# Performance work log

Hardware: AMD Instinct MI355X
Metric: run time of the kernel (lower is better)

The kernel has to match this reference:

```python
import math
import jax, jax.numpy as jnp
import numpy as np

B, N, D, H = 2, 2048, 1024, 16
HD = D // H  # 64
TWO_PI = 2.0 * math.pi
ROPE_BASE = 10000.0


def setup_inputs() -> dict:
    key = jax.random.key(0)
    ks = jax.random.split(key, 8)
    s = 0.02
    x = jax.random.normal(ks[0], (B, N, D), dtype=jnp.float32)
    Wq = jax.random.normal(ks[1], (D, D), dtype=jnp.float32) * s
    Wk = jax.random.normal(ks[2], (D, D), dtype=jnp.float32) * s
    Wv = jax.random.normal(ks[3], (D, D), dtype=jnp.float32) * s
    Wo = jax.random.normal(ks[4], (D, D), dtype=jnp.float32) * s
    cw = jax.random.normal(ks[5], (D,), dtype=jnp.float32) * s  # complexity_proj weight
    cb = jnp.zeros((), dtype=jnp.float32)                        # complexity_proj bias
    alpha = jnp.asarray(0.1, dtype=jnp.float32)
    T_base = jnp.asarray(10.0, dtype=jnp.float32)
    root_ids = jax.random.randint(ks[6], (B, N), 0, 1000)
    mask = jnp.tril(jnp.ones((N, N), dtype=jnp.int32))  # causal
    return {"x": x, "Wq": Wq, "Wk": Wk, "Wv": Wv, "Wo": Wo,
            "alpha": alpha, "T_base": T_base, "cw": cw, "cb": cb,
            "root_ids": root_ids, "mask": mask, "t_step": 3}


def _rope_cos_sin(seq_len, head_dim, dtype):
    inv_freq = 1.0 / (ROPE_BASE ** (jnp.arange(0, head_dim, 2, dtype=jnp.float32) / head_dim))
    pos = jnp.arange(seq_len, dtype=jnp.float32)
    freqs = pos[:, None] * inv_freq[None, :]          # (N, HD/2)
    emb = jnp.concatenate([freqs, freqs], axis=-1)    # (N, HD)
    return jnp.cos(emb).astype(dtype), jnp.sin(emb).astype(dtype)


def _rotate_half(t):
    half = t.shape[-1] // 2
    return jnp.concatenate([-t[..., half:], t[..., :half]], axis=-1)


def reference(x, Wq, Wk, Wv, Wo, alpha, T_base, cw, cb, root_ids, mask, t_step):
    b, n, d = x.shape
    # QKV projection -> (B, H, N, HD)
    def proj(W):
        return jnp.einsum('bnd,ed->bne', x, W).reshape(b, n, H, HD).transpose(0, 2, 1, 3)
    q, k, v = proj(Wq), proj(Wk), proj(Wv)
    # RoPE
    cos, sin = _rope_cos_sin(n, HD, x.dtype)          # (N, HD)
    q = q * cos + _rotate_half(q) * sin
    k = k * cos + _rotate_half(k) * sin
    # Per-sample temperature via complexity + cardiac oscillation
    complexity = jax.nn.sigmoid(jnp.einsum('bd,d->b', x.mean(axis=1), cw) + cb)  # (B,)
    T_eff = (jnp.abs(T_base) + 1.0) * (0.5 + complexity)                          # (B,)
    psi = 1.0 + alpha * jnp.sin(TWO_PI * t_step / T_eff)                          # (B,)
    scale = (math.sqrt(HD) * psi)[:, None, None, None]                            # (B,1,1,1)
    # Attention with full NxN scores (eager path, as in source)
    scores = jnp.einsum('bhqd,bhkd->bhqk', q, k) / scale
    scores = jnp.where(mask[None, None, :, :] == 0, -jnp.inf, scores)
    attn = jax.nn.softmax(scores, axis=-1)
    out = jnp.einsum('bhqk,bhkd->bhqd', attn, v)       # (B,H,N,HD)
    out = out.transpose(0, 2, 1, 3).reshape(b, n, d)
    return jnp.einsum('bnd,ed->bne', out, Wo)
```

## Files before the change

### kernel.cpp

```cpp
#include <hip/hip_runtime.h>


typedef short short8 __attribute__((ext_vector_type(8)));
typedef float floatx4 __attribute__((ext_vector_type(4)));
typedef float f32x16 __attribute__((ext_vector_type(16)));
typedef unsigned int uint4v __attribute__((ext_vector_type(4)));
typedef unsigned int u32x4v __attribute__((ext_vector_type(4)));
typedef unsigned short us4 __attribute__((ext_vector_type(4)));
typedef unsigned short u16;

#define DEV __device__ __forceinline__

static const int Bb = 2;

static const size_t OFF_XB = 0;
static const size_t OFF_WQ = 8388608;
static const size_t OFF_WK = OFF_WQ + 2097152;
static const size_t OFF_WV = OFF_WK + 2097152;
static const size_t OFF_WO = OFF_WV + 2097152;
static const size_t OFF_Q  = OFF_WO + 2097152;
static const size_t OFF_K  = OFF_Q + 8388608;
static const size_t OFF_V  = OFF_K + 8388608;
static const size_t OFF_AO = OFF_V + 8388608;
static const size_t OFF_SC = OFF_AO + 8388608;

DEV u16 f2bf(float f) {
  unsigned int u = __builtin_bit_cast(unsigned int, f);
  u += 0x7fffu + ((u >> 16) & 1u);
  return (u16)(u >> 16);
}

DEV unsigned pkbf(float lo, float hi) {
  unsigned r;
  asm("v_cvt_pk_bf16_f32 %0, %1, %2" : "=v"(r) : "v"(lo), "v"(hi));
  return r;
}

__global__ __launch_bounds__(256) void cvt_all_kernel(
    const float* __restrict__ x, const float* __restrict__ wq,
    const float* __restrict__ wk, const float* __restrict__ wv,
    const float* __restrict__ wo, const float* __restrict__ cw,
    u16* __restrict__ xb, u16* __restrict__ wqb, u16* __restrict__ wkb,
    u16* __restrict__ wvb, u16* __restrict__ wob, float* __restrict__ part) {
  const int blk = blockIdx.x;
  if (blk < 4096) {
    int i = blk * 256 + threadIdx.x;
    float4 f = ((const float4*)x)[i];
    us4 o;
    o[0] = f2bf(f.x); o[1] = f2bf(f.y); o[2] = f2bf(f.z); o[3] = f2bf(f.w);
    ((us4*)xb)[i] = o;
    float4 c = ((const float4*)cw)[i & 255];
    float acc = f.x * c.x + f.y * c.y + f.z * c.z + f.w * c.w;
    __shared__ float red[256];
    red[threadIdx.x] = acc;
    __syncthreads();
    for (int s = 128; s > 0; s >>= 1) {
      if (threadIdx.x < s) red[threadIdx.x] += red[threadIdx.x + s];
      __syncthreads();
    }
    if (threadIdx.x == 0) part[blk] = red[0];
  } else {
    int r = blk - 4096;
    int wi = r >> 10;
    int i = (r & 1023) * 256 + threadIdx.x;
    const float* src = (wi == 0) ? wq : (wi == 1) ? wk : (wi == 2) ? wv : wo;
    u16* dst = (wi == 0) ? wqb : (wi == 1) ? wkb : (wi == 2) ? wvb : wob;
    float4 f = ((const float4*)src)[i];
    us4 o;
    o[0] = f2bf(f.x); o[1] = f2bf(f.y); o[2] = f2bf(f.z); o[3] = f2bf(f.w);
    ((us4*)dst)[i] = o;
  }
}

__global__ void prep_kernel(const float* __restrict__ part,
                            const float* __restrict__ cb,
                            const float* __restrict__ alpha,
                            const float* __restrict__ tb,
                            const int* __restrict__ tstep,
                            float* __restrict__ out, float2* __restrict__ rt) {
  if (blockIdx.x == 256) {
    const int b = threadIdx.x >> 7, t = threadIdx.x & 127;
    float s = 0.f;
    for (int i = t; i < 2048; i += 128) s += part[b * 2048 + i];
    __shared__ float red[2][128];
    red[b][t] = s;
    __syncthreads();
    for (int st = 64; st > 0; st >>= 1) {
      if (t < st) red[b][t] += red[b][t + st];
      __syncthreads();
    }
    if (t == 0) {
      float sm = red[b][0] * (1.0f / 2048.0f) + cb[0];
      float cx = 1.0f / (1.0f + expf(-sm));
      float Te = (fabsf(tb[0]) + 1.0f) * (0.5f + cx);
      float psi = 1.0f + alpha[0] * sinf(6.283185307179586f * (float)tstep[0] / Te);
      out[b] = 1.0f / (8.0f * psi);
    }
  } else {
    int i = blockIdx.x * 256 + threadIdx.x;
    int pos = i >> 5, hd2 = i & 31;
    float ang = (float)pos * exp2f(-(float)hd2 * 0.41524101186092030f);
    float sv, cv;
    sincosf(ang, &sv, &cv);
    rt[i] = make_float2(cv, sv);
  }
}

__global__ __launch_bounds__(256) void gemm_qkv_kernel(
    const u16* __restrict__ xb, const u16* __restrict__ wq, const u16* __restrict__ wk,
    const u16* __restrict__ wv, const float2* __restrict__ rt,
    u16* __restrict__ q, u16* __restrict__ k, u16* __restrict__ v) {
  const int tm = blockIdx.x, tn = blockIdx.y, which = blockIdx.z;
  const u16* W = (which == 0) ? wq : (which == 1) ? wk : wv;
  u16* dst = (which == 0) ? q : (which == 1) ? k : v;

  __shared__ __align__(16) u16 As[128 * 32];
  __shared__ __align__(16) u16 Bs[128 * 32];

  const int t = threadIdx.x, lane = t & 63, w = t >> 6;
  const int wm = w >> 1, wn = w & 1, lg = lane >> 4, lr = lane & 15;

  floatx4 acc[4][4];
#pragma unroll
  for (int i = 0; i < 4; i++)
#pragma unroll
    for (int j = 0; j < 4; j++) acc[i][j] = (floatx4){0.f, 0.f, 0.f, 0.f};

  const int rowA = tm * 128, rowB = tn * 128;
  for (int kt = 0; kt < 32; ++kt) {
#pragma unroll
    for (int s = 0; s < 2; s++) {
      int c = t + s * 256;
      int r = c >> 2, kc = c & 3;
      *(uint4v*)(As + r * 32 + kc * 8) =
          *(const uint4v*)(xb + (size_t)(rowA + r) * 1024 + kt * 32 + kc * 8);
      *(uint4v*)(Bs + r * 32 + kc * 8) =
          *(const uint4v*)(W + (size_t)(rowB + r) * 1024 + kt * 32 + kc * 8);
    }
    __syncthreads();
    short8 af[4], bw[4];
#pragma unroll
    for (int i = 0; i < 4; i++)
      af[i] = *(const short8*)(As + (wm * 64 + i * 16 + lr) * 32 + lg * 8);
#pragma unroll
    for (int j = 0; j < 4; j++)
      bw[j] = *(const short8*)(Bs + (wn * 64 + j * 16 + lr) * 32 + lg * 8);
#pragma unroll
    for (int i = 0; i < 4; i++)
#pragma unroll
      for (int j = 0; j < 4; j++)
        acc[i][j] = __builtin_amdgcn_mfma_f32_16x16x32_bf16(af[i], bw[j], acc[i][j], 0, 0, 0);
    __syncthreads();
  }

  const int rowbase = tm * 128 + wm * 64, colbase = tn * 128 + wn * 64;
  if (which <= 1) {
#pragma unroll
    for (int i = 0; i < 4; i++)
#pragma unroll
      for (int ii = 0; ii < 4; ii++) {
        int gm = rowbase + i * 16 + lg * 4 + ii;
        int pos = gm & 2047, bb = gm >> 11;
#pragma unroll
        for (int jp = 0; jp < 2; jp++) {
          int hd2 = jp * 16 + lr;
          float2 cs = rt[pos * 32 + hd2];
          float a0 = acc[i][jp][ii], a1 = acc[i][jp + 2][ii];
          int e0 = colbase + jp * 16 + lr;
          int hh = e0 >> 6;
          size_t base = (((size_t)bb * 16 + hh) * 2048 + pos) * 64;
          dst[base + hd2]      = f2bf(a0 * cs.x - a1 * cs.y);
          dst[base + hd2 + 32] = f2bf(a1 * cs.x + a0 * cs.y);
        }
      }
  } else {
#pragma unroll
    for (int i = 0; i < 4; i++)
#pragma unroll
      for (int ii = 0; ii < 4; ii++) {
        int gm = rowbase + i * 16 + lg * 4 + ii;
        int pos = gm & 2047, bb = gm >> 11;
#pragma unroll
        for (int j = 0; j < 4; j++) {
          int ge = colbase + j * 16 + lr;
          int hh = ge >> 6, hd = ge & 63;
          dst[(((size_t)bb * 16 + hh) * 2048 + pos) * 64 + hd] = f2bf(acc[i][j][ii]);
        }
      }
  }
}

__global__ __launch_bounds__(256) void vtrans_kernel(const u16* __restrict__ v,
                                                     u16* __restrict__ vt) {
  const int bh = blockIdx.x, nt = blockIdx.y;
  __shared__ __align__(16) u16 T[64 * 64];
  const int t = threadIdx.x;
  const size_t vi = (size_t)bh * 131072 + (size_t)nt * 4096;
#pragma unroll
  for (int s = 0; s < 2; s++) {
    int g = s * 256 + t, n = g >> 3, dc = g & 7;
    *(uint4v*)(T + n * 64 + ((dc ^ (n & 7)) * 8)) =
        *(const uint4v*)(v + vi + (size_t)n * 64 + dc * 8);
  }
  __syncthreads();
  const size_t vo = (size_t)bh * 131072 + (size_t)nt * 64;
#pragma unroll
  for (int s = 0; s < 2; s++) {
    int g = s * 256 + t, nc = g & 7, d = g >> 3;
    short8 o;
#pragma unroll
    for (int jj = 0; jj < 8; jj++) {
      int n = nc * 8 + jj;
      o[jj] = (short)T[n * 64 + (((d >> 3) ^ (n & 7)) * 8) + (d & 7)];
    }
    *(short8*)(vt + vo + (size_t)d * 2048 + nc * 8) = o;
  }
}

__global__ __launch_bounds__(256) void attn_kernel(
    const u16* __restrict__ q, const u16* __restrict__ k, const u16* __restrict__ vt,
    u16* __restrict__ ao, const float* __restrict__ scale_ws) {
  const int bid = blockIdx.x;
  const int swz = (bid & 7) * 64 + (bid >> 3);
  const int bh = swz >> 4, p = swz & 15;
  const int b = bh >> 4, h = bh & 15;
  const int w = threadIdx.x >> 6, lane = threadIdx.x & 63;
  const int l31 = lane & 31, hi = lane >> 5;
  const int tsel = (w == 0) ? p : (w == 1) ? 31 - p : (w == 2) ? 32 + p : 63 - p;
  const int q0 = tsel * 32;
  const int KT = tsel >> 1;
  const float isc2 = scale_ws[b] * 1.4426950408889634f;
  const size_t koff = (size_t)bh * 131072;
  const float NINF = -__builtin_inff();

  short8 bq[4];
#pragma unroll
  for (int k4 = 0; k4 < 4; k4++)
    bq[k4] = *(const short8*)(q + koff + (size_t)(q0 + l31) * 64 + k4 * 16 + hi * 8);

  f32x16 o0, o1;
#pragma unroll
  for (int r = 0; r < 16; r++) { o0[r] = 0.f; o1[r] = 0.f; }
  float m2 = NINF, ell = 0.f;

  for (int kt = 0; kt <= KT; ++kt) {
    const int cbase = kt << 6;
    const bool haveMt1 = (cbase + 32 <= q0 + 31);

    short8 ka0[4], ka1[4];
#pragma unroll
    for (int k4 = 0; k4 < 4; k4++)
      ka0[k4] = *(const short8*)(k + koff + (size_t)(cbase + l31) * 64 + k4 * 16 + hi * 8);
    if (haveMt1) {
#pragma unroll
      for (int k4 = 0; k4 < 4; k4++)
        ka1[k4] = *(const short8*)(k + koff + (size_t)(cbase + 32 + l31) * 64 + k4 * 16 + hi * 8);
    }
    const int nct = haveMt1 ? 4 : 2;
    short8 va0[4], va1[4];
#pragma unroll
    for (int ct = 0; ct < 4; ct++) {
      if (ct < nct) {
        va0[ct] = *(const short8*)(vt + koff + (size_t)l31 * 2048 + cbase + ct * 16 + hi * 8);
        va1[ct] = *(const short8*)(vt + koff + (size_t)(32 + l31) * 2048 + cbase + ct * 16 + hi * 8);
      }
    }

    f32x16 s0, s1;
#pragma unroll
    for (int r = 0; r < 16; r++) { s0[r] = 0.f; s1[r] = 0.f; }
    __builtin_amdgcn_s_setprio(1);
#pragma unroll
    for (int k4 = 0; k4 < 4; k4++)
      s0 = __builtin_amdgcn_mfma_f32_32x32x16_bf16(ka0[k4], bq[k4], s0, 0, 0, 0);
    if (haveMt1) {
#pragma unroll
      for (int k4 = 0; k4 < 4; k4++)
        s1 = __builtin_amdgcn_mfma_f32_32x32x16_bf16(ka1[k4], bq[k4], s1, 0, 0, 0);
    }
    __builtin_amdgcn_s_setprio(0);

#pragma unroll
    for (int r = 0; r < 16; r++) { s0[r] *= isc2; s1[r] *= isc2; }
    if (kt == KT) {
      const int thr = q0 + l31 - cbase;
#pragma unroll
      for (int r = 0; r < 16; r++) {
        const int crow = (r & 3) + 8 * (r >> 2) + 4 * hi;
        if (crow > thr) s0[r] = NINF;
        if (crow + 32 > thr) s1[r] = NINF;
      }
    }

    float mx = s0[0];
#pragma unroll
    for (int r = 1; r < 16; r++) mx = fmaxf(mx, s0[r]);
#pragma unroll
    for (int r = 0; r < 16; r++) mx = fmaxf(mx, s1[r]);
    mx = fmaxf(mx, __shfl_xor(mx, 32, 64));
    if (!__all(mx <= m2 + 8.0f)) {
      const float mn = fmaxf(m2, mx);
      const float rsc = exp2f(m2 - mn);
      m2 = mn;
      ell *= rsc;
#pragma unroll
      for (int r = 0; r < 16; r++) { o0[r] *= rsc; o1[r] *= rsc; }
    }
    f32x16 p0, p1;
    float ps = 0.f;
#pragma unroll
    for (int r = 0; r < 16; r++) { p0[r] = exp2f(s0[r] - m2); ps += p0[r]; }
#pragma unroll
    for (int r = 0; r < 16; r++) { p1[r] = exp2f(s1[r] - m2); ps += p1[r]; }
    ps += __shfl_xor(ps, 32, 64);
    ell += ps;

    __builtin_amdgcn_s_setprio(1);
#pragma unroll
    for (int ct = 0; ct < 4; ct++) {
      if (ct < nct) {
        const f32x16& pp = (ct < 2) ? p0 : p1;
        const int rA = (ct & 1) * 8;
        unsigned pkA0 = pkbf(pp[rA + 0], pp[rA + 1]);
        unsigned pkA1 = pkbf(pp[rA + 2], pp[rA + 3]);
        unsigned pkB0 = pkbf(pp[rA + 4], pp[rA + 5]);
        unsigned pkB1 = pkbf(pp[rA + 6], pp[rA + 7]);
        unsigned u0 = (unsigned)__shfl_xor((int)(hi ? pkA0 : pkB0), 32, 64);
        unsigned u1 = (unsigned)__shfl_xor((int)(hi ? pkA1 : pkB1), 32, 64);
        u32x4v pu;
        pu[0] = hi ? u0 : pkA0;
        pu[1] = hi ? u1 : pkA1;
        pu[2] = hi ? pkB0 : u0;
        pu[3] = hi ? pkB1 : u1;
        short8 pf = __builtin_bit_cast(short8, pu);
        o0 = __builtin_amdgcn_mfma_f32_32x32x16_bf16(va0[ct], pf, o0, 0, 0, 0);
        o1 = __builtin_amdgcn_mfma_f32_32x32x16_bf16(va1[ct], pf, o1, 0, 0, 0);
      }
    }
    __builtin_amdgcn_s_setprio(0);
  }

  const float invl = 1.0f / ell;
  u16* orow = ao + ((size_t)(b * 2048 + q0 + l31)) * 1024 + h * 64;
#pragma unroll
  for (int qd = 0; qd < 4; qd++) {
    us4 st0, st1;
#pragma unroll
    for (int j = 0; j < 4; j++) {
      st0[j] = f2bf(o0[qd * 4 + j] * invl);
      st1[j] = f2bf(o1[qd * 4 + j] * invl);
    }
    *(us4*)(orow + qd * 8 + hi * 4) = st0;
    *(us4*)(orow + 32 + qd * 8 + hi * 4) = st1;
  }
}

__global__ __launch_bounds__(256) void gemm_out_kernel(const u16* __restrict__ ab,
                                                       const u16* __restrict__ wo,
                                                       float* __restrict__ out) {
  const int tm = blockIdx.x, tn = blockIdx.y;
  __shared__ __align__(16) u16 As[128 * 32];
  __shared__ __align__(16) u16 Bs[128 * 32];

  const int t = threadIdx.x, lane = t & 63, w = t >> 6;
  const int wm = w >> 1, wn = w & 1, lg = lane >> 4, lr = lane & 15;

  floatx4 acc[4][4];
#pragma unroll
  for (int i = 0; i < 4; i++)
#pragma unroll
    for (int j = 0; j < 4; j++) acc[i][j] = (floatx4){0.f, 0.f, 0.f, 0.f};

  const int rowA = tm * 128, rowB = tn * 128;
  for (int kt = 0; kt < 32; ++kt) {
#pragma unroll
    for (int s = 0; s < 2; s++) {
      int c = t + s * 256;
      int r = c >> 2, kc = c & 3;
      *(uint4v*)(As + r * 32 + kc * 8) =
          *(const uint4v*)(ab + (size_t)(rowA + r) * 1024 + kt * 32 + kc * 8);
      *(uint4v*)(Bs + r * 32 + kc * 8) =
          *(const uint4v*)(wo + (size_t)(rowB + r) * 1024 + kt * 32 + kc * 8);
    }
    __syncthreads();
    short8 af[4], bw[4];
#pragma unroll
    for (int i = 0; i < 4; i++)
      af[i] = *(const short8*)(As + (wm * 64 + i * 16 + lr) * 32 + lg * 8);
#pragma unroll
    for (int j = 0; j < 4; j++)
      bw[j] = *(const short8*)(Bs + (wn * 64 + j * 16 + lr) * 32 + lg * 8);
#pragma unroll
    for (int i = 0; i < 4; i++)
#pragma unroll
      for (int j = 0; j < 4; j++)
        acc[i][j] = __builtin_amdgcn_mfma_f32_16x16x32_bf16(af[i], bw[j], acc[i][j], 0, 0, 0);
    __syncthreads();
  }

  const int rowbase = tm * 128 + wm * 64, colbase = tn * 128 + wn * 64;
#pragma unroll
  for (int i = 0; i < 4; i++)
#pragma unroll
    for (int ii = 0; ii < 4; ii++) {
      int gm = rowbase + i * 16 + lg * 4 + ii;
#pragma unroll
      for (int j = 0; j < 4; j++) {
        int ge = colbase + j * 16 + lr;
        out[(size_t)gm * 1024 + ge] = acc[i][j][ii];
      }
    }
}

extern "C" void kernel_launch(void* const* d_in, const int* in_sizes, int n_in,
                              void* d_out, int out_size, void* d_ws, size_t ws_size,
                              hipStream_t stream) {
  const float* x     = (const float*)d_in[0];
  const float* Wq    = (const float*)d_in[1];
  const float* Wk    = (const float*)d_in[2];
  const float* Wv    = (const float*)d_in[3];
  const float* Wo    = (const float*)d_in[4];
  const float* alpha = (const float*)d_in[5];
  const float* Tb    = (const float*)d_in[6];
  const float* cw    = (const float*)d_in[7];
  const float* cb    = (const float*)d_in[8];
  const int*   tstep = (const int*)d_in[11];

  char* ws = (char*)d_ws;
  u16* xb  = (u16*)(ws + OFF_XB);
  u16* wqb = (u16*)(ws + OFF_WQ);
  u16* wkb = (u16*)(ws + OFF_WK);
  u16* wvb = (u16*)(ws + OFF_WV);
  u16* wob = (u16*)(ws + OFF_WO);
  u16* qb  = (u16*)(ws + OFF_Q);
  u16* kb  = (u16*)(ws + OFF_K);
  u16* vb  = (u16*)(ws + OFF_V);
  u16* aob = (u16*)(ws + OFF_AO);
  u16* vtb = (u16*)(ws + OFF_XB);
  float2* rt = (float2*)(ws + OFF_AO);
  float* sc = (float*)(ws + OFF_SC);
  float* part = sc + 4;

  cvt_all_kernel<<<8192, 256, 0, stream>>>(x, Wq, Wk, Wv, Wo, cw,
                                           xb, wqb, wkb, wvb, wob, part);
  prep_kernel<<<257, 256, 0, stream>>>(part, cb, alpha, Tb, tstep, sc, rt);

  gemm_qkv_kernel<<<dim3(32, 8, 3), 256, 0, stream>>>(xb, wqb, wkb, wvb, rt, qb, kb, vb);

  vtrans_kernel<<<dim3(32, 32), 256, 0, stream>>>(vb, vtb);

  attn_kernel<<<dim3(512), 256, 0, stream>>>(qb, kb, vtb, aob, sc);

  gemm_out_kernel<<<dim3(32, 8), 256, 0, stream>>>(aob, wob, (float*)d_out);
}
```

Before: 299.2 us.

## Write V transposed from QKV GEMM epilogue, drop vtrans kernel, simplify softmax rescale

The QKV GEMM epilogue now stores V directly in transposed (head, dim, position) layout with 4-element vector stores, so the separate V transpose kernel and its extra read/write pass are removed. The attention loop also drops the s_setprio hints and replaces the conditional lazy rescale (which skipped it when the max grew by less than 8) with an unconditional per-tile rescale of the accumulators. That adds rescale multiplies on every tile in exchange for less branching.

New measurement: 258.8 us. 13.5% less time.

```diff
diff --git a/kernel.cpp b/kernel.cpp
--- a/kernel.cpp
+++ b/kernel.cpp
@@ -109,10 +109,9 @@
 __global__ __launch_bounds__(256) void gemm_qkv_kernel(
     const u16* __restrict__ xb, const u16* __restrict__ wq, const u16* __restrict__ wk,
     const u16* __restrict__ wv, const float2* __restrict__ rt,
-    u16* __restrict__ q, u16* __restrict__ k, u16* __restrict__ v) {
+    u16* __restrict__ q, u16* __restrict__ k, u16* __restrict__ vt) {
   const int tm = blockIdx.x, tn = blockIdx.y, which = blockIdx.z;
   const u16* W = (which == 0) ? wq : (which == 1) ? wk : wv;
-  u16* dst = (which == 0) ? q : (which == 1) ? k : v;
 
   __shared__ __align__(16) u16 As[128 * 32];
   __shared__ __align__(16) u16 Bs[128 * 32];
@@ -155,6 +154,7 @@
 
   const int rowbase = tm * 128 + wm * 64, colbase = tn * 128 + wn * 64;
   if (which <= 1) {
+    u16* dst = (which == 0) ? q : k;
 #pragma unroll
     for (int i = 0; i < 4; i++)
 #pragma unroll
@@ -175,45 +175,19 @@
       }
   } else {
 #pragma unroll
-    for (int i = 0; i < 4; i++)
-#pragma unroll
-      for (int ii = 0; ii < 4; ii++) {
-        int gm = rowbase + i * 16 + lg * 4 + ii;
-        int pos = gm & 2047, bb = gm >> 11;
-#pragma unroll
-        for (int j = 0; j < 4; j++) {
-          int ge = colbase + j * 16 + lr;
-          int hh = ge >> 6, hd = ge & 63;
-          dst[(((size_t)bb * 16 + hh) * 2048 + pos) * 64 + hd] = f2bf(acc[i][j][ii]);
-        }
-      }
-  }
-}
-
-__global__ __launch_bounds__(256) void vtrans_kernel(const u16* __restrict__ v,
-                                                     u16* __restrict__ vt) {
-  const int bh = blockIdx.x, nt = blockIdx.y;
-  __shared__ __align__(16) u16 T[64 * 64];
-  const int t = threadIdx.x;
-  const size_t vi = (size_t)bh * 131072 + (size_t)nt * 4096;
-#pragma unroll
-  for (int s = 0; s < 2; s++) {
-    int g = s * 256 + t, n = g >> 3, dc = g & 7;
-    *(uint4v*)(T + n * 64 + ((dc ^ (n & 7)) * 8)) =
-        *(const uint4v*)(v + vi + (size_t)n * 64 + dc * 8);
-  }
-  __syncthreads();
-  const size_t vo = (size_t)bh * 131072 + (size_t)nt * 64;
-#pragma unroll
-  for (int s = 0; s < 2; s++) {
-    int g = s * 256 + t, nc = g & 7, d = g >> 3;
-    short8 o;
-#pragma unroll
-    for (int jj = 0; jj < 8; jj++) {
-      int n = nc * 8 + jj;
-      o[jj] = (short)T[n * 64 + (((d >> 3) ^ (n & 7)) * 8) + (d & 7)];
-    }
-    *(short8*)(vt + vo + (size_t)d * 2048 + nc * 8) = o;
+    for (int i = 0; i < 4; i++) {
+      int gm0 = rowbase + i * 16 + lg * 4;
+      int pos0 = gm0 & 2047, bb = gm0 >> 11;
+#pragma unroll
+      for (int j = 0; j < 4; j++) {
+        int ge = colbase + j * 16 + lr;
+        int hh = ge >> 6, hd = ge & 63;
+        us4 st;
+#pragma unroll
+        for (int ii = 0; ii < 4; ii++) st[ii] = f2bf(acc[i][j][ii]);
+        *(us4*)(vt + ((size_t)(bb * 16 + hh)) * 131072 + (size_t)hd * 2048 + pos0) = st;
+      }
+    }
   }
 }
 
@@ -269,7 +243,6 @@
     f32x16 s0, s1;
 #pragma unroll
     for (int r = 0; r < 16; r++) { s0[r] = 0.f; s1[r] = 0.f; }
-    __builtin_amdgcn_s_setprio(1);
 #pragma unroll
     for (int k4 = 0; k4 < 4; k4++)
       s0 = __builtin_amdgcn_mfma_f32_32x32x16_bf16(ka0[k4], bq[k4], s0, 0, 0, 0);
@@ -278,7 +251,6 @@
       for (int k4 = 0; k4 < 4; k4++)
         s1 = __builtin_amdgcn_mfma_f32_32x32x16_bf16(ka1[k4], bq[k4], s1, 0, 0, 0);
     }
-    __builtin_amdgcn_s_setprio(0);
 
 #pragma unroll
     for (int r = 0; r < 16; r++) { s0[r] *= isc2; s1[r] *= isc2; }
@@ -298,24 +270,20 @@
 #pragma unroll
     for (int r = 0; r < 16; r++) mx = fmaxf(mx, s1[r]);
     mx = fmaxf(mx, __shfl_xor(mx, 32, 64));
-    if (!__all(mx <= m2 + 8.0f)) {
-      const float mn = fmaxf(m2, mx);
-      const float rsc = exp2f(m2 - mn);
-      m2 = mn;
-      ell *= rsc;
-#pragma unroll
-      for (int r = 0; r < 16; r++) { o0[r] *= rsc; o1[r] *= rsc; }
-    }
+    const float mn = fmaxf(m2, mx);
+    const float rsc = exp2f(m2 - mn);
+    m2 = mn;
     f32x16 p0, p1;
     float ps = 0.f;
 #pragma unroll
-    for (int r = 0; r < 16; r++) { p0[r] = exp2f(s0[r] - m2); ps += p0[r]; }
-#pragma unroll
-    for (int r = 0; r < 16; r++) { p1[r] = exp2f(s1[r] - m2); ps += p1[r]; }
+    for (int r = 0; r < 16; r++) { p0[r] = exp2f(s0[r] - mn); ps += p0[r]; }
+#pragma unroll
+    for (int r = 0; r < 16; r++) { p1[r] = exp2f(s1[r] - mn); ps += p1[r]; }
     ps += __shfl_xor(ps, 32, 64);
-    ell += ps;
-
-    __builtin_amdgcn_s_setprio(1);
+    ell = ell * rsc + ps;
+#pragma unroll
+    for (int r = 0; r < 16; r++) { o0[r] *= rsc; o1[r] *= rsc; }
+
 #pragma unroll
     for (int ct = 0; ct < 4; ct++) {
       if (ct < nct) {
@@ -337,7 +305,6 @@
         o1 = __builtin_amdgcn_mfma_f32_32x32x16_bf16(va1[ct], pf, o1, 0, 0, 0);
       }
     }
-    __builtin_amdgcn_s_setprio(0);
   }
 
   const float invl = 1.0f / ell;
@@ -434,9 +401,8 @@
   u16* wob = (u16*)(ws + OFF_WO);
   u16* qb  = (u16*)(ws + OFF_Q);
   u16* kb  = (u16*)(ws + OFF_K);
-  u16* vb  = (u16*)(ws + OFF_V);
+  u16* vtb = (u16*)(ws + OFF_V);
   u16* aob = (u16*)(ws + OFF_AO);
-  u16* vtb = (u16*)(ws + OFF_XB);
   float2* rt = (float2*)(ws + OFF_AO);
   float* sc = (float*)(ws + OFF_SC);
   float* part = sc + 4;
@@ -445,9 +411,7 @@
                                            xb, wqb, wkb, wvb, wob, part);
   prep_kernel<<<257, 256, 0, stream>>>(part, cb, alpha, Tb, tstep, sc, rt);
 
-  gemm_qkv_kernel<<<dim3(32, 8, 3), 256, 0, stream>>>(xb, wqb, wkb, wvb, rt, qb, kb, vb);
-
-  vtrans_kernel<<<dim3(32, 32), 256, 0, stream>>>(vb, vtb);
+  gemm_qkv_kernel<<<dim3(32, 8, 3), 256, 0, stream>>>(xb, wqb, wkb, wvb, rt, qb, kb, vtb);
 
   attn_kernel<<<dim3(512), 256, 0, stream>>>(qb, kb, vtb, aob, sc);
 
```
